# Kernel optimization log

Hardware: AMD Instinct MI355X
Metric: run time of the kernel (lower is better)

## Reference

```python
import jax, jax.numpy as jnp
import numpy as np
from jax import lax

THRESH = 1.0
TAU = 2.0
DECAY = 1.0 - 1.0 / TAU      # 0.5
INPUT_SCALE = 1.0 / TAU      # 0.5


def setup_inputs() -> dict:
    key = jax.random.key(0)
    # x: [T, B, C, H, W]
    x = jax.random.normal(key, (16, 32, 128, 32, 32), dtype=jnp.float32)
    return {"x": x}


def reference(x):
    # LIF neuron scan over time: mem decays, adds scaled input, spikes above
    # threshold, hard-resets to 0 where it spiked.
    def step(mem, xt):
        u1 = mem * DECAY + xt * INPUT_SCALE          # membrane before spike
        spike = (u1 > THRESH).astype(xt.dtype)
        mem_next = u1 * (1.0 - spike)                # reset where spiked
        return mem_next, spike

    mem0 = jnp.zeros_like(x[0])
    _, spikes = lax.scan(step, mem0, x)
    return spikes  # [T, B, C, H, W]
```

## Files before the change

kernel.cpp:

```cpp
#include <hip/hip_runtime.h>


constexpr int   T_STEPS     = 16;
constexpr int   COLS        = 4;
constexpr float DECAY       = 0.5f;
constexpr float INPUT_SCALE = 0.5f;
constexpr float THRESH      = 1.0f;

typedef float floatx4 __attribute__((ext_vector_type(4)));

__global__ __launch_bounds__(256) void lif_scan_kernel(
    const float* __restrict__ x,
    float*       __restrict__ out,
    int n_per_t)
{
    const int n4 = n_per_t >> 2;
    const int f4_base = blockIdx.x * (256 * COLS) + threadIdx.x;

    const floatx4* __restrict__ xin  = reinterpret_cast<const floatx4*>(x);
    floatx4*       __restrict__ outv = reinterpret_cast<floatx4*>(out);

    floatx4 mem[COLS];
    #pragma unroll
    for (int c = 0; c < COLS; ++c) mem[c] = (floatx4)(0.f);

    #pragma unroll
    for (int t = 0; t < T_STEPS; ++t) {
        const size_t slice = (size_t)t * (size_t)n4 + (size_t)f4_base;

        floatx4 v[COLS];
        #pragma unroll
        for (int c = 0; c < COLS; ++c)
            v[c] = xin[slice + c * 256];

        #pragma unroll
        for (int c = 0; c < COLS; ++c) {
            floatx4 u, s;
            #pragma unroll
            for (int k = 0; k < 4; ++k) {
                u[k]      = mem[c][k] * DECAY + v[c][k] * INPUT_SCALE;
                s[k]      = (u[k] > THRESH) ? 1.0f : 0.0f;
                mem[c][k] = (u[k] > THRESH) ? 0.0f : u[k];
            }
            outv[slice + c * 256] = s;
        }
    }
}

extern "C" void kernel_launch(void* const* d_in, const int* in_sizes, int n_in,
                              void* d_out, int out_size, void* d_ws, size_t ws_size,
                              hipStream_t stream) {
    const float* x   = (const float*)d_in[0];
    float*       out = (float*)d_out;

    const int total   = in_sizes[0];
    const int n_per_t = total / T_STEPS;

    const int threads = 256;
    const int n4      = n_per_t / 4;
    const int blocks  = n4 / (threads * COLS);

    lif_scan_kernel<<<blocks, threads, 0, stream>>>(x, out, n_per_t);
}
```

Before: 429.0 us.

## Prefetch all timesteps per thread with nontemporal loads/stores, one float4 per thread

Each thread now handles a single float4 column and issues all 16 timestep loads up front, using nontemporal load and store builtins, before running the scan in registers. The grid grows fourfold, since the four-columns-per-thread scheme is gone. The aim is more memory-level parallelism per thread and less cache pollution for this streaming, bandwidth-bound kernel. In exchange it holds 64 floats of input per thread in registers and adds a launch_bounds occupancy hint.

```diff
diff --git a/kernel.cpp b/kernel.cpp
--- a/kernel.cpp
+++ b/kernel.cpp
@@ -2,48 +2,40 @@
 
 
 constexpr int   T_STEPS     = 16;
-constexpr int   COLS        = 4;
 constexpr float DECAY       = 0.5f;
 constexpr float INPUT_SCALE = 0.5f;
 constexpr float THRESH      = 1.0f;
 
 typedef float floatx4 __attribute__((ext_vector_type(4)));
 
-__global__ __launch_bounds__(256) void lif_scan_kernel(
+__global__ __launch_bounds__(256, 2) void lif_scan_kernel(
     const float* __restrict__ x,
     float*       __restrict__ out,
-    int n_per_t)
+    int n4)
 {
-    const int n4 = n_per_t >> 2;
-    const int f4_base = blockIdx.x * (256 * COLS) + threadIdx.x;
+    const int idx = blockIdx.x * 256 + threadIdx.x;
 
-    const floatx4* __restrict__ xin  = reinterpret_cast<const floatx4*>(x);
-    floatx4*       __restrict__ outv = reinterpret_cast<floatx4*>(out);
+    const floatx4* __restrict__ xv  = reinterpret_cast<const floatx4*>(x);
+    floatx4*       __restrict__ ov  = reinterpret_cast<floatx4*>(out);
 
-    floatx4 mem[COLS];
+    floatx4 v[T_STEPS];
     #pragma unroll
-    for (int c = 0; c < COLS; ++c) mem[c] = (floatx4)(0.f);
+    for (int t = 0; t < T_STEPS; ++t)
+        v[t] = __builtin_nontemporal_load(&xv[(size_t)t * (size_t)n4 + (size_t)idx]);
 
+    asm volatile("" ::: "memory");
+
+    floatx4 mem = (floatx4)(0.f);
     #pragma unroll
     for (int t = 0; t < T_STEPS; ++t) {
-        const size_t slice = (size_t)t * (size_t)n4 + (size_t)f4_base;
-
-        floatx4 v[COLS];
+        floatx4 s;
         #pragma unroll
-        for (int c = 0; c < COLS; ++c)
-            v[c] = xin[slice + c * 256];
-
-        #pragma unroll
-        for (int c = 0; c < COLS; ++c) {
-            floatx4 u, s;
-            #pragma unroll
-            for (int k = 0; k < 4; ++k) {
-                u[k]      = mem[c][k] * DECAY + v[c][k] * INPUT_SCALE;
-                s[k]      = (u[k] > THRESH) ? 1.0f : 0.0f;
-                mem[c][k] = (u[k] > THRESH) ? 0.0f : u[k];
-            }
-            outv[slice + c * 256] = s;
+        for (int k = 0; k < 4; ++k) {
+            const float u = mem[k] * DECAY + v[t][k] * INPUT_SCALE;
+            s[k]   = (u > THRESH) ? 1.0f : 0.0f;
+            mem[k] = (u > THRESH) ? 0.0f : u;
         }
+        __builtin_nontemporal_store(s, &ov[(size_t)t * (size_t)n4 + (size_t)idx]);
     }
 }
 
@@ -55,10 +47,10 @@
 
     const int total   = in_sizes[0];
     const int n_per_t = total / T_STEPS;
+    const int n4      = n_per_t / 4;
 
     const int threads = 256;
-    const int n4      = n_per_t / 4;
-    const int blocks  = n4 / (threads * COLS);
+    const int blocks  = n4 / threads;
 
-    lif_scan_kernel<<<blocks, threads, 0, stream>>>(x, out, n_per_t);
+    lif_scan_kernel<<<blocks, threads, 0, stream>>>(x, out, n4);
 }
```

Result: slower. 446.9 us (+4.2%).
